# Optimization experiments

Hardware: AMD Instinct MI355X
Metric: run time of the kernel (lower is better)

Reference implementation:

```python
import jax, jax.numpy as jnp
import numpy as np

N, E = 50000, 800000
F_IN, HID, SENT = 128, 128, 128
NEG_SLOPE = 0.2  # GATConv default negative_slope


def _glorot(key, shape):
    fan_in, fan_out = shape[0], shape[-1]
    lim = float(np.sqrt(6.0 / (fan_in + fan_out)))
    return jax.random.uniform(key, shape, jnp.float32, -lim, lim)


def _gat_layer(x, src, dst, edge_attr, W, att_s, att_d, We, att_e, b):
    """PyG GATConv, heads=1, add_self_loops=True (fill_value='mean')."""
    n = x.shape[0]
    # self-loop edge_attr = mean of incoming edge features per dst node
    deg = jax.ops.segment_sum(jnp.ones(src.shape[0], x.dtype), dst, num_segments=n)
    loop_attr = jax.ops.segment_sum(edge_attr, dst, num_segments=n) / jnp.maximum(deg, 1.0)[:, None]
    loops = jnp.arange(n, dtype=src.dtype)
    src = jnp.concatenate([src, loops])
    dst = jnp.concatenate([dst, loops])
    ea = jnp.concatenate([edge_attr, loop_attr], axis=0)
    # projections (lin_src used for both src and dst when x is a single tensor)
    h = x @ W                           # [N, C]
    a_s = h @ att_s                     # [N]
    a_d = h @ att_d                     # [N]
    a_e = (ea @ We) @ att_e             # [E+N]
    alpha = jax.nn.leaky_relu(a_s[src] + a_d[dst] + a_e, NEG_SLOPE)
    # segment softmax over dst neighborhoods (self-loops guarantee nonempty)
    m = jax.ops.segment_max(alpha, dst, num_segments=n)
    ex = jnp.exp(alpha - m[dst])
    w = ex / jax.ops.segment_sum(ex, dst, num_segments=n)[dst]
    # message = alpha * h_src, scatter-add to dst
    return jax.ops.segment_sum(w[:, None] * h[src], dst, num_segments=n) + b


def setup_inputs() -> dict:
    key = jax.random.key(0)
    ks = jax.random.split(key, 16)
    x = jax.random.normal(ks[0], (N, F_IN), jnp.float32)
    edge_index = jax.random.randint(ks[1], (2, E), 0, N, jnp.int64)
    edge_attr = jax.random.normal(ks[2], (E, SENT), jnp.float32)
    params = {
        'W1': _glorot(ks[3], (F_IN, HID)),
        'a1s': _glorot(ks[4], (HID,)),
        'a1d': _glorot(ks[5], (HID,)),
        'We1': _glorot(ks[6], (SENT, HID)),
        'ae1': _glorot(ks[7], (HID,)),
        'b1': jnp.zeros((HID,), jnp.float32),
        'W2': _glorot(ks[8], (HID, HID)),
        'a2s': _glorot(ks[9], (HID,)),
        'a2d': _glorot(ks[10], (HID,)),
        'We2': _glorot(ks[11], (SENT, HID)),
        'ae2': _glorot(ks[12], (HID,)),
        'b2': jnp.zeros((HID,), jnp.float32),
    }
    return {'x': x, 'edge_index': edge_index, 'edge_attr': edge_attr, **params}


def reference(x, edge_index, edge_attr, W1, a1s, a1d, We1, ae1, b1,
              W2, a2s, a2d, We2, ae2, b2):
    src, dst = edge_index[0], edge_index[1]
    h = _gat_layer(x, src, dst, edge_attr, W1, a1s, a1d, We1, ae1, b1)
    h = jax.nn.relu(h)  # dropout p=0.1 inactive in eval
    return _gat_layer(h, src, dst, edge_attr, W2, a2s, a2d, We2, ae2, b2)
```

## Files before the change

kernel.cpp:

```cpp
#include <hip/hip_runtime.h>
#include <cstdint>

#define D 128
#define NEG 0.2f

typedef __attribute__((ext_vector_type(8))) short bf16x8;
typedef __attribute__((ext_vector_type(4))) float f32x4;

__device__ __forceinline__ float wsum(float v){
#pragma unroll
  for(int m=32;m;m>>=1) v += __shfl_xor(v,m,64);
  return v;
}
__device__ __forceinline__ float lrelu(float a){ return a>0.f ? a : NEG*a; }
__device__ __forceinline__ unsigned short f2bf(float f){
  unsigned int u = __float_as_uint(f);
  u += 0x7fffu + ((u>>16)&1u);
  return (unsigned short)(u>>16);
}
__device__ __forceinline__ float bf2f(unsigned short s){
  return __uint_as_float(((unsigned int)s)<<16);
}

__global__ __launch_bounds__(256) void k_init(const float* __restrict__ We1, const float* __restrict__ ae1,
                                              const float* __restrict__ We2, const float* __restrict__ ae2,
                                              const float* __restrict__ W1,  const float* __restrict__ W2,
                                              float* __restrict__ weae, ushort* __restrict__ Wtb){
  __shared__ ushort lds[16][128];
  if (blockIdx.x < 64){
    int gw  = (blockIdx.x*256 + threadIdx.x) >> 6;
    int lane = threadIdx.x & 63;
    const float* We = (gw & 128) ? We2 : We1;
    const float* ae = (gw & 128) ? ae2 : ae1;
    int row = gw & 127;
    float2 v = ((const float2*)(We + (size_t)row*D))[lane];
    float2 a = ((const float2*)ae)[lane];
    float p = wsum(v.x*a.x + v.y*a.y);
    if (!lane) weae[gw] = p;
  } else {
    int b = blockIdx.x - 64;
    int layer = b >> 3;
    int kb = (b & 7) * 16;
    const float* W = layer ? W2 : W1;
    int t = threadIdx.x;
#pragma unroll
    for (int p = 0; p < 8; ++p){
      int idx = t + p*256;
      int kl = idx >> 7, c = idx & 127;
      lds[kl][c] = f2bf(W[(size_t)(kb+kl)*128 + c]);
    }
    __syncthreads();
    int c = t >> 1, kc = (t & 1) * 8;
    ushort tmp[8];
#pragma unroll
    for (int m = 0; m < 8; ++m) tmp[m] = lds[kc+m][c];
    *(uint4*)&Wtb[(size_t)layer*16384 + (size_t)c*128 + kb + kc] = *(uint4*)tmp;
  }
}

__global__ __launch_bounds__(256) void k_edge(const float* __restrict__ EA, const int* __restrict__ dstv,
                                              const float* __restrict__ weae,
                                              float2* __restrict__ aeE12,
                                              int* __restrict__ deg, int E){
  int l   = threadIdx.x & 63;
  int sub = l & 7;
  int grp = l >> 3;
  float4 w1v[4], w2v[4];
#pragma unroll
  for (int k = 0; k < 4; ++k){
    w1v[k] = ((const float4*)weae)[sub + 8*k];
    w2v[k] = ((const float4*)weae)[32 + sub + 8*k];
  }
  int gwave  = (blockIdx.x*blockDim.x + threadIdx.x) >> 6;
  int nwaves = (gridDim.x*blockDim.x) >> 6;
  for (int e0 = gwave*8; e0 < E; e0 += nwaves*8){
    int e = e0 + grp;
    const float4* row = (const float4*)(EA + (size_t)e*D);
    float s1 = 0.f, s2 = 0.f;
#pragma unroll
    for (int k = 0; k < 4; ++k){
      float4 v = row[sub + 8*k];
      s1 += v.x*w1v[k].x + v.y*w1v[k].y + v.z*w1v[k].z + v.w*w1v[k].w;
      s2 += v.x*w2v[k].x + v.y*w2v[k].y + v.z*w2v[k].z + v.w*w2v[k].w;
    }
#pragma unroll
    for (int m = 1; m <= 4; m <<= 1){
      s1 += __shfl_xor(s1, m, 64);
      s2 += __shfl_xor(s2, m, 64);
    }
    if (!sub){
      aeE12[e] = make_float2(s1, s2);
      atomicAdd(deg + dstv[e], 1);
    }
  }
}

__global__ __launch_bounds__(256) void k_scan1(const int* __restrict__ deg, int* __restrict__ bsum, int N){
  __shared__ int s[256];
  int i = blockIdx.x*256 + threadIdx.x;
  s[threadIdx.x] = (i < N) ? deg[i] : 0;
  __syncthreads();
#pragma unroll
  for (int st = 128; st; st >>= 1){
    if (threadIdx.x < st) s[threadIdx.x] += s[threadIdx.x + st];
    __syncthreads();
  }
  if (!threadIdx.x) bsum[blockIdx.x] = s[0];
}
__global__ __launch_bounds__(256) void k_scan2(const int* __restrict__ bsum, int* __restrict__ boff, int NB){
  __shared__ int s[256];
  int t = threadIdx.x;
  int v = (t < NB) ? bsum[t] : 0;
  s[t] = v; __syncthreads();
  for (int d = 1; d < 256; d <<= 1){
    int x = (t >= d) ? s[t-d] : 0;
    __syncthreads();
    s[t] += x;
    __syncthreads();
  }
  boff[t] = s[t] - v;
}
__global__ __launch_bounds__(256) void k_scan3(const int* __restrict__ deg, const int* __restrict__ boff,
                                               int* __restrict__ rowp, int N, int E){
  __shared__ int s[256];
  int t = threadIdx.x;
  int i = blockIdx.x*256 + t;
  int v = (i < N) ? deg[i] : 0;
  s[t] = v; __syncthreads();
  for (int d = 1; d < 256; d <<= 1){
    int x = (t >= d) ? s[t-d] : 0;
    __syncthreads();
    s[t] += x;
    __syncthreads();
  }
  if (i < N) rowp[i] = boff[blockIdx.x] + s[t] - v;
  if (i == N-1) rowp[N] = E;
}

__global__ __launch_bounds__(256) void k_csr(const int* __restrict__ srcv, const int* __restrict__ dstv,
                                             const int* __restrict__ rowp, int* __restrict__ cursor,
                                             const float2* __restrict__ aeE12,
                                             int4* __restrict__ csr, int E){
  int e = blockIdx.x*256 + threadIdx.x;
  if (e >= E) return;
  int d = dstv[e];
  int pos = rowp[d] + atomicAdd(cursor + d, 1);
  float2 ae = aeE12[e];
  int4 rec;
  rec.x = srcv[e];
  rec.y = __float_as_int(ae.x);
  rec.z = __float_as_int(ae.y);
  rec.w = d;
  csr[pos] = rec;
}

__global__ __launch_bounds__(256) void k_gemm(const float* __restrict__ Xf, const ushort* __restrict__ Xb,
                                              const ushort* __restrict__ Wtb,
                                              const float* __restrict__ atts, const float* __restrict__ attd,
                                              ushort* __restrict__ Hb,
                                              float* __restrict__ a_s, float* __restrict__ a_d, int N){
  __shared__ ushort xsb[64*136];
  __shared__ ushort wsb[128*136];
  int tid = threadIdx.x;
  int rowbase = blockIdx.x*64;
  if (Xf){
#pragma unroll
    for (int i = 0; i < 4; ++i){
      int idx = tid + i*256;
      int r = idx >> 4, ch = idx & 15;
      int gr = rowbase + r;
      int grc = (gr < N) ? gr : 0;
      const float4* src = (const float4*)(Xf + (size_t)grc*128 + ch*8);
      float4 a = src[0], b = src[1];
      uint4 o;
      o.x = (unsigned)f2bf(a.x) | ((unsigned)f2bf(a.y)<<16);
      o.y = (unsigned)f2bf(a.z) | ((unsigned)f2bf(a.w)<<16);
      o.z = (unsigned)f2bf(b.x) | ((unsigned)f2bf(b.y)<<16);
      o.w = (unsigned)f2bf(b.z) | ((unsigned)f2bf(b.w)<<16);
      *(uint4*)&xsb[r*136 + ch*8] = o;
    }
  } else {
#pragma unroll
    for (int i = 0; i < 4; ++i){
      int idx = tid + i*256;
      int r = idx >> 4, ch = idx & 15;
      int gr = rowbase + r;
      int grc = (gr < N) ? gr : 0;
      *(uint4*)&xsb[r*136 + ch*8] = *(const uint4*)&Xb[(size_t)grc*128 + ch*8];
    }
  }
#pragma unroll
  for (int i = 0; i < 8; ++i){
    int idx = tid + i*256;
    int c = idx >> 4, ch = idx & 15;
    *(uint4*)&wsb[c*136 + ch*8] = *(const uint4*)&Wtb[(size_t)c*128 + ch*8];
  }
  __syncthreads();

  int lane = tid & 63;
  int w    = tid >> 6;
  int l15  = lane & 15;
  int lg   = lane >> 4;
  int r0   = w*16;

  f32x4 acc[8];
#pragma unroll
  for (int ct = 0; ct < 8; ++ct) acc[ct] = (f32x4){0.f,0.f,0.f,0.f};

#pragma unroll
  for (int ks = 0; ks < 4; ++ks){
    bf16x8 af = *(const bf16x8*)&xsb[(r0 + l15)*136 + ks*32 + lg*8];
#pragma unroll
    for (int ct = 0; ct < 8; ++ct){
      bf16x8 bfr = *(const bf16x8*)&wsb[(ct*16 + l15)*136 + ks*32 + lg*8];
      acc[ct] = __builtin_amdgcn_mfma_f32_16x16x32_bf16(af, bfr, acc[ct], 0, 0, 0);
    }
  }

  float attsv[8], attdv[8];
#pragma unroll
  for (int ct = 0; ct < 8; ++ct){
    attsv[ct] = atts[ct*16 + l15];
    attdv[ct] = attd[ct*16 + l15];
  }
  float ps[4] = {0,0,0,0}, pd[4] = {0,0,0,0};
#pragma unroll
  for (int ct = 0; ct < 8; ++ct)
#pragma unroll
    for (int j = 0; j < 4; ++j){
      ps[j] += acc[ct][j]*attsv[ct];
      pd[j] += acc[ct][j]*attdv[ct];
    }
#pragma unroll
  for (int m = 1; m <= 8; m <<= 1)
#pragma unroll
    for (int j = 0; j < 4; ++j){
      ps[j] += __shfl_xor(ps[j], m, 64);
      pd[j] += __shfl_xor(pd[j], m, 64);
    }
#pragma unroll
  for (int j = 0; j < 4; ++j){
    int gr = rowbase + r0 + lg*4 + j;
    if (gr < N && l15 == 0){
      a_s[gr] = ps[j];
      a_d[gr] = pd[j];
    }
  }
#pragma unroll
  for (int ct = 0; ct < 8; ++ct)
#pragma unroll
    for (int j = 0; j < 4; ++j){
      int r = r0 + lg*4 + j;
      xsb[r*136 + ct*16 + l15] = f2bf(acc[ct][j]);
    }
  __syncthreads();
#pragma unroll
  for (int i = 0; i < 4; ++i){
    int idx = tid + i*256;
    int r = idx >> 4, ch = idx & 15;
    int gr = rowbase + r;
    if (gr < N)
      *(uint4*)&Hb[(size_t)gr*128 + ch*8] = *(const uint4*)&xsb[r*136 + ch*8];
  }
}

__global__ __launch_bounds__(256) void k_aggr(const ushort* __restrict__ Hb,
                                              const float* __restrict__ a_s, const float* __restrict__ a_d,
                                              const int* __restrict__ rowp, const int4* __restrict__ csr,
                                              int layer,
                                              const float* __restrict__ bias,
                                              float* __restrict__ OUTF, ushort* __restrict__ OUTB, int N){
  __shared__ uint2 lse[4][64];
  int wslot = threadIdx.x >> 6;
  int wid  = (blockIdx.x*blockDim.x + threadIdx.x) >> 6;
  int lane = threadIdx.x & 63;
  if (wid >= N) return;
  int p0 = rowp[wid], p1 = rowp[wid+1];
  float as_own = a_s[wid];
  float ad     = a_d[wid];
  int l32 = lane & 31;
  int hw  = lane >> 5;
  ushort4 uself = make_ushort4(0,0,0,0);
  if (!hw) uself = *(const ushort4*)(Hb + (size_t)wid*D + l32*4);
  float denom = 0.f, sumae = 0.f;
  float4 acc = {0.f,0.f,0.f,0.f};
  for (int c0 = p0; c0 < p1; c0 += 64){
    int p = c0 + lane;
    bool valid = p < p1;
    int4 rec = valid ? csr[p] : make_int4(0,0,0,0);
    float ae = valid ? __int_as_float(layer ? rec.z : rec.y) : 0.f;
    float ex = valid ? __expf(lrelu(a_s[rec.x] + ad + ae)) : 0.f;
    sumae += wsum(ae);
    denom += wsum(ex);
    lse[wslot][lane] = make_uint2((unsigned)rec.x, __float_as_uint(ex));
    int cnt = p1 - c0; if (cnt > 64) cnt = 64;
    for (int it = 0; it*16 < cnt; ++it){
      int base = it*16 + hw*8;
#pragma unroll
      for (int k = 0; k < 8; ++k){
        uint2 t = lse[wslot][base + k];
        float w2 = __uint_as_float(t.y);
        ushort4 u = *(const ushort4*)(Hb + (size_t)t.x*D + l32*4);
        acc.x += w2*bf2f(u.x); acc.y += w2*bf2f(u.y);
        acc.z += w2*bf2f(u.z); acc.w += w2*bf2f(u.w);
      }
    }
  }
  float dg = (float)(p1 - p0);
  float la = sumae / fmaxf(dg, 1.0f);
  float ex_self = __expf(lrelu(as_own + ad + la));
  denom += ex_self;
  acc.x += __shfl_xor(acc.x, 32);
  acc.y += __shfl_xor(acc.y, 32);
  acc.z += __shfl_xor(acc.z, 32);
  acc.w += __shfl_xor(acc.w, 32);
  if (!hw){
    acc.x += ex_self*bf2f(uself.x); acc.y += ex_self*bf2f(uself.y);
    acc.z += ex_self*bf2f(uself.z); acc.w += ex_self*bf2f(uself.w);
    float4 bv = *(const float4*)(bias + l32*4);
    float inv = 1.0f/denom;
    float ox = acc.x*inv + bv.x, oy = acc.y*inv + bv.y;
    float oz = acc.z*inv + bv.z, ow = acc.w*inv + bv.w;
    if (OUTB){
      ox=fmaxf(ox,0.f); oy=fmaxf(oy,0.f); oz=fmaxf(oz,0.f); ow=fmaxf(ow,0.f);
      ushort4 o;
      o.x=f2bf(ox); o.y=f2bf(oy); o.z=f2bf(oz); o.w=f2bf(ow);
      *(ushort4*)(OUTB + (size_t)wid*D + l32*4) = o;
    } else {
      *(float4*)(OUTF + (size_t)wid*D + l32*4) = make_float4(ox,oy,oz,ow);
    }
  }
}

extern "C" void kernel_launch(void* const* d_in, const int* in_sizes, int n_in,
                              void* d_out, int out_size, void* d_ws, size_t ws_size,
                              hipStream_t stream){
  (void)n_in; (void)out_size; (void)ws_size;
  const float* x   = (const float*)d_in[0];
  const int*   ei  = (const int*)d_in[1];
  const float* ea  = (const float*)d_in[2];
  const float* W1  = (const float*)d_in[3];
  const float* a1s = (const float*)d_in[4];
  const float* a1d = (const float*)d_in[5];
  const float* We1 = (const float*)d_in[6];
  const float* ae1 = (const float*)d_in[7];
  const float* b1  = (const float*)d_in[8];
  const float* W2  = (const float*)d_in[9];
  const float* a2s = (const float*)d_in[10];
  const float* a2d = (const float*)d_in[11];
  const float* We2 = (const float*)d_in[12];
  const float* ae2 = (const float*)d_in[13];
  const float* b2  = (const float*)d_in[14];
  int N = in_sizes[0] / D;
  int E = in_sizes[1] / 2;
  const int* srcv = ei;
  const int* dstv = ei + E;
  float* out = (float*)d_out;

  char* p = (char*)d_ws;
  auto allocB = [&](size_t bytes)->void*{
    void* r = (void*)p; p += (bytes + 255) & ~(size_t)255; return r;
  };
  int* deg     = (int*)allocB((size_t)N*4);
  int* cursor  = (int*)allocB((size_t)N*4);
  char* zero_end = p;
  ushort* hb   = (ushort*)allocB((size_t)N*D*2);
  ushort* x2b  = (ushort*)allocB((size_t)N*D*2);
  ushort* Wtb  = (ushort*)allocB((size_t)2*128*128*2);
  float* aeE12 = (float*)allocB((size_t)E*8);
  int4* csr    = (int4*)allocB((size_t)E*16);
  float* as_   = (float*)allocB((size_t)N*4);
  float* ad_   = (float*)allocB((size_t)N*4);
  float* weae  = (float*)allocB(1024);
  int* rowp    = (int*)allocB((size_t)(N+1)*4);
  int* bsum    = (int*)allocB(1024);
  int* boff    = (int*)allocB(1024);

  hipMemsetAsync(deg, 0, (size_t)(zero_end - (char*)deg), stream);

  k_init<<<80,256,0,stream>>>(We1,ae1,We2,ae2,W1,W2,weae,Wtb);
  k_edge<<<2048,256,0,stream>>>(ea,dstv,weae,(float2*)aeE12,deg,E);

  int nb = (N + 255)/256;
  k_scan1<<<nb,256,0,stream>>>(deg,bsum,N);
  k_scan2<<<1,256,0,stream>>>(bsum,boff,nb);
  k_scan3<<<nb,256,0,stream>>>(deg,boff,rowp,N,E);
  k_csr<<<(E+255)/256,256,0,stream>>>(srcv,dstv,rowp,cursor,(const float2*)aeE12,csr,E);

  int gemmb = (N + 63)/64;
  int wgrid = (N + 3)/4;

  k_gemm<<<gemmb,256,0,stream>>>(x, nullptr, Wtb,          a1s, a1d, hb, as_, ad_, N);
  k_aggr<<<wgrid,256,0,stream>>>(hb, as_, ad_, rowp, csr, 0, b1, nullptr, x2b, N);

  k_gemm<<<gemmb,256,0,stream>>>(nullptr, x2b, Wtb + 16384, a2s, a2d, hb, as_, ad_, N);
  k_aggr<<<wgrid,256,0,stream>>>(hb, as_, ad_, rowp, csr, 1, b2, out, nullptr, N);
}
```

Before: 271.4 us.

## Reorder CSR build: histogram first, fuse edge projection with CSR scatter into per-layer lists

The degree histogram now runs as its own kernel first. The first scan level is merged with the weight-prep kernel, and scan levels two and three are combined into one kernel. The edge projection kernel now scatters directly into CSR position, writing two compact per-layer (src, ae) 8-byte lists instead of an intermediate aeE12 array plus a 16-byte CSR record. This removes one kernel pass over E edges and halves the per-edge record read in each aggregation layer, at the cost of random scatter writes from the edge-attribute kernel.

```diff
diff --git a/kernel.cpp b/kernel.cpp
--- a/kernel.cpp
+++ b/kernel.cpp
@@ -22,13 +22,31 @@
   return __uint_as_float(((unsigned int)s)<<16);
 }
 
-__global__ __launch_bounds__(256) void k_init(const float* __restrict__ We1, const float* __restrict__ ae1,
-                                              const float* __restrict__ We2, const float* __restrict__ ae2,
-                                              const float* __restrict__ W1,  const float* __restrict__ W2,
-                                              float* __restrict__ weae, ushort* __restrict__ Wtb){
+__global__ __launch_bounds__(256) void k_hist(const int* __restrict__ dstv, int* __restrict__ deg, int E){
+  int e = blockIdx.x*256 + threadIdx.x;
+  if (e < E) atomicAdd(deg + dstv[e], 1);
+}
+
+__global__ __launch_bounds__(256) void k_scan1i(const int* __restrict__ deg, int* __restrict__ bsum, int N, int NB,
+                                                const float* __restrict__ We1, const float* __restrict__ ae1,
+                                                const float* __restrict__ We2, const float* __restrict__ ae2,
+                                                const float* __restrict__ W1,  const float* __restrict__ W2,
+                                                float* __restrict__ weae, ushort* __restrict__ Wtb){
+  __shared__ int s[256];
   __shared__ ushort lds[16][128];
-  if (blockIdx.x < 64){
-    int gw  = (blockIdx.x*256 + threadIdx.x) >> 6;
+  int b = blockIdx.x;
+  if (b < NB){
+    int i = b*256 + threadIdx.x;
+    s[threadIdx.x] = (i < N) ? deg[i] : 0;
+    __syncthreads();
+#pragma unroll
+    for (int st = 128; st; st >>= 1){
+      if (threadIdx.x < st) s[threadIdx.x] += s[threadIdx.x + st];
+      __syncthreads();
+    }
+    if (!threadIdx.x) bsum[b] = s[0];
+  } else if (b < NB + 64){
+    int gw  = ((b - NB)*256 + threadIdx.x) >> 6;
     int lane = threadIdx.x & 63;
     const float* We = (gw & 128) ? We2 : We1;
     const float* ae = (gw & 128) ? ae2 : ae1;
@@ -38,9 +56,9 @@
     float p = wsum(v.x*a.x + v.y*a.y);
     if (!lane) weae[gw] = p;
   } else {
-    int b = blockIdx.x - 64;
-    int layer = b >> 3;
-    int kb = (b & 7) * 16;
+    int bb = b - NB - 64;
+    int layer = bb >> 3;
+    int kb = (bb & 7) * 16;
     const float* W = layer ? W2 : W1;
     int t = threadIdx.x;
 #pragma unroll
@@ -58,56 +76,8 @@
   }
 }
 
-__global__ __launch_bounds__(256) void k_edge(const float* __restrict__ EA, const int* __restrict__ dstv,
-                                              const float* __restrict__ weae,
-                                              float2* __restrict__ aeE12,
-                                              int* __restrict__ deg, int E){
-  int l   = threadIdx.x & 63;
-  int sub = l & 7;
-  int grp = l >> 3;
-  float4 w1v[4], w2v[4];
-#pragma unroll
-  for (int k = 0; k < 4; ++k){
-    w1v[k] = ((const float4*)weae)[sub + 8*k];
-    w2v[k] = ((const float4*)weae)[32 + sub + 8*k];
-  }
-  int gwave  = (blockIdx.x*blockDim.x + threadIdx.x) >> 6;
-  int nwaves = (gridDim.x*blockDim.x) >> 6;
-  for (int e0 = gwave*8; e0 < E; e0 += nwaves*8){
-    int e = e0 + grp;
-    const float4* row = (const float4*)(EA + (size_t)e*D);
-    float s1 = 0.f, s2 = 0.f;
-#pragma unroll
-    for (int k = 0; k < 4; ++k){
-      float4 v = row[sub + 8*k];
-      s1 += v.x*w1v[k].x + v.y*w1v[k].y + v.z*w1v[k].z + v.w*w1v[k].w;
-      s2 += v.x*w2v[k].x + v.y*w2v[k].y + v.z*w2v[k].z + v.w*w2v[k].w;
-    }
-#pragma unroll
-    for (int m = 1; m <= 4; m <<= 1){
-      s1 += __shfl_xor(s1, m, 64);
-      s2 += __shfl_xor(s2, m, 64);
-    }
-    if (!sub){
-      aeE12[e] = make_float2(s1, s2);
-      atomicAdd(deg + dstv[e], 1);
-    }
-  }
-}
-
-__global__ __launch_bounds__(256) void k_scan1(const int* __restrict__ deg, int* __restrict__ bsum, int N){
-  __shared__ int s[256];
-  int i = blockIdx.x*256 + threadIdx.x;
-  s[threadIdx.x] = (i < N) ? deg[i] : 0;
-  __syncthreads();
-#pragma unroll
-  for (int st = 128; st; st >>= 1){
-    if (threadIdx.x < st) s[threadIdx.x] += s[threadIdx.x + st];
-    __syncthreads();
-  }
-  if (!threadIdx.x) bsum[blockIdx.x] = s[0];
-}
-__global__ __launch_bounds__(256) void k_scan2(const int* __restrict__ bsum, int* __restrict__ boff, int NB){
+__global__ __launch_bounds__(256) void k_scan23(const int* __restrict__ deg, const int* __restrict__ bsum,
+                                                int* __restrict__ rowp, int NB, int N, int E){
   __shared__ int s[256];
   int t = threadIdx.x;
   int v = (t < NB) ? bsum[t] : 0;
@@ -118,40 +88,61 @@
     s[t] += x;
     __syncthreads();
   }
-  boff[t] = s[t] - v;
-}
-__global__ __launch_bounds__(256) void k_scan3(const int* __restrict__ deg, const int* __restrict__ boff,
-                                               int* __restrict__ rowp, int N, int E){
-  __shared__ int s[256];
-  int t = threadIdx.x;
+  int boff = (blockIdx.x == 0) ? 0 : s[blockIdx.x - 1];
+  __syncthreads();
   int i = blockIdx.x*256 + t;
-  int v = (i < N) ? deg[i] : 0;
-  s[t] = v; __syncthreads();
+  int dv = (i < N) ? deg[i] : 0;
+  s[t] = dv; __syncthreads();
   for (int d = 1; d < 256; d <<= 1){
     int x = (t >= d) ? s[t-d] : 0;
     __syncthreads();
     s[t] += x;
     __syncthreads();
   }
-  if (i < N) rowp[i] = boff[blockIdx.x] + s[t] - v;
+  if (i < N) rowp[i] = boff + s[t] - dv;
   if (i == N-1) rowp[N] = E;
 }
 
-__global__ __launch_bounds__(256) void k_csr(const int* __restrict__ srcv, const int* __restrict__ dstv,
-                                             const int* __restrict__ rowp, int* __restrict__ cursor,
-                                             const float2* __restrict__ aeE12,
-                                             int4* __restrict__ csr, int E){
-  int e = blockIdx.x*256 + threadIdx.x;
-  if (e >= E) return;
-  int d = dstv[e];
-  int pos = rowp[d] + atomicAdd(cursor + d, 1);
-  float2 ae = aeE12[e];
-  int4 rec;
-  rec.x = srcv[e];
-  rec.y = __float_as_int(ae.x);
-  rec.z = __float_as_int(ae.y);
-  rec.w = d;
-  csr[pos] = rec;
+__global__ __launch_bounds__(256) void k_edge(const float* __restrict__ EA,
+                                              const int* __restrict__ srcv, const int* __restrict__ dstv,
+                                              const float* __restrict__ weae,
+                                              const int* __restrict__ rowp, int* __restrict__ cursor,
+                                              uint2* __restrict__ pl1, uint2* __restrict__ pl2, int E){
+  int l   = threadIdx.x & 63;
+  int sub = l & 7;
+  int grp = l >> 3;
+  float4 w1v[4], w2v[4];
+#pragma unroll
+  for (int k = 0; k < 4; ++k){
+    w1v[k] = ((const float4*)weae)[sub + 8*k];
+    w2v[k] = ((const float4*)weae)[32 + sub + 8*k];
+  }
+  int gwave  = (blockIdx.x*blockDim.x + threadIdx.x) >> 6;
+  int nwaves = (gridDim.x*blockDim.x) >> 6;
+  for (int e0 = gwave*8; e0 < E; e0 += nwaves*8){
+    int e = e0 + grp;
+    if (e >= E) continue;
+    const float4* row = (const float4*)(EA + (size_t)e*D);
+    float s1 = 0.f, s2 = 0.f;
+#pragma unroll
+    for (int k = 0; k < 4; ++k){
+      float4 v = row[sub + 8*k];
+      s1 += v.x*w1v[k].x + v.y*w1v[k].y + v.z*w1v[k].z + v.w*w1v[k].w;
+      s2 += v.x*w2v[k].x + v.y*w2v[k].y + v.z*w2v[k].z + v.w*w2v[k].w;
+    }
+#pragma unroll
+    for (int m = 1; m <= 4; m <<= 1){
+      s1 += __shfl_xor(s1, m, 64);
+      s2 += __shfl_xor(s2, m, 64);
+    }
+    if (!sub){
+      int d = dstv[e];
+      int pos = rowp[d] + atomicAdd(cursor + d, 1);
+      unsigned s = (unsigned)srcv[e];
+      pl1[pos] = make_uint2(s, __float_as_uint(s1));
+      pl2[pos] = make_uint2(s, __float_as_uint(s2));
+    }
+  }
 }
 
 __global__ __launch_bounds__(256) void k_gemm(const float* __restrict__ Xf, const ushort* __restrict__ Xb,
@@ -266,8 +257,7 @@
 
 __global__ __launch_bounds__(256) void k_aggr(const ushort* __restrict__ Hb,
                                               const float* __restrict__ a_s, const float* __restrict__ a_d,
-                                              const int* __restrict__ rowp, const int4* __restrict__ csr,
-                                              int layer,
+                                              const int* __restrict__ rowp, const uint2* __restrict__ pl,
                                               const float* __restrict__ bias,
                                               float* __restrict__ OUTF, ushort* __restrict__ OUTB, int N){
   __shared__ uint2 lse[4][64];
@@ -287,12 +277,12 @@
   for (int c0 = p0; c0 < p1; c0 += 64){
     int p = c0 + lane;
     bool valid = p < p1;
-    int4 rec = valid ? csr[p] : make_int4(0,0,0,0);
-    float ae = valid ? __int_as_float(layer ? rec.z : rec.y) : 0.f;
+    uint2 rec = valid ? pl[p] : make_uint2(0u, 0u);
+    float ae = valid ? __uint_as_float(rec.y) : 0.f;
     float ex = valid ? __expf(lrelu(a_s[rec.x] + ad + ae)) : 0.f;
     sumae += wsum(ae);
     denom += wsum(ex);
-    lse[wslot][lane] = make_uint2((unsigned)rec.x, __float_as_uint(ex));
+    lse[wslot][lane] = make_uint2(rec.x, __float_as_uint(ex));
     int cnt = p1 - c0; if (cnt > 64) cnt = 64;
     for (int it = 0; it*16 < cnt; ++it){
       int base = it*16 + hw*8;
@@ -367,32 +357,28 @@
   ushort* hb   = (ushort*)allocB((size_t)N*D*2);
   ushort* x2b  = (ushort*)allocB((size_t)N*D*2);
   ushort* Wtb  = (ushort*)allocB((size_t)2*128*128*2);
-  float* aeE12 = (float*)allocB((size_t)E*8);
-  int4* csr    = (int4*)allocB((size_t)E*16);
+  uint2* pl1   = (uint2*)allocB((size_t)E*8);
+  uint2* pl2   = (uint2*)allocB((size_t)E*8);
   float* as_   = (float*)allocB((size_t)N*4);
   float* ad_   = (float*)allocB((size_t)N*4);
   float* weae  = (float*)allocB(1024);
   int* rowp    = (int*)allocB((size_t)(N+1)*4);
   int* bsum    = (int*)allocB(1024);
-  int* boff    = (int*)allocB(1024);
 
   hipMemsetAsync(deg, 0, (size_t)(zero_end - (char*)deg), stream);
 
-  k_init<<<80,256,0,stream>>>(We1,ae1,We2,ae2,W1,W2,weae,Wtb);
-  k_edge<<<2048,256,0,stream>>>(ea,dstv,weae,(float2*)aeE12,deg,E);
-
   int nb = (N + 255)/256;
-  k_scan1<<<nb,256,0,stream>>>(deg,bsum,N);
-  k_scan2<<<1,256,0,stream>>>(bsum,boff,nb);
-  k_scan3<<<nb,256,0,stream>>>(deg,boff,rowp,N,E);
-  k_csr<<<(E+255)/256,256,0,stream>>>(srcv,dstv,rowp,cursor,(const float2*)aeE12,csr,E);
+  k_hist  <<<(E+255)/256,256,0,stream>>>(dstv, deg, E);
+  k_scan1i<<<nb+80,256,0,stream>>>(deg, bsum, N, nb, We1,ae1,We2,ae2,W1,W2, weae, Wtb);
+  k_scan23<<<nb,256,0,stream>>>(deg, bsum, rowp, nb, N, E);
+  k_edge  <<<2048,256,0,stream>>>(ea, srcv, dstv, weae, rowp, cursor, pl1, pl2, E);
 
   int gemmb = (N + 63)/64;
   int wgrid = (N + 3)/4;
 
   k_gemm<<<gemmb,256,0,stream>>>(x, nullptr, Wtb,          a1s, a1d, hb, as_, ad_, N);
-  k_aggr<<<wgrid,256,0,stream>>>(hb, as_, ad_, rowp, csr, 0, b1, nullptr, x2b, N);
+  k_aggr<<<wgrid,256,0,stream>>>(hb, as_, ad_, rowp, pl1, b1, nullptr, x2b, N);
 
   k_gemm<<<gemmb,256,0,stream>>>(nullptr, x2b, Wtb + 16384, a2s, a2d, hb, as_, ad_, N);
-  k_aggr<<<wgrid,256,0,stream>>>(hb, as_, ad_, rowp, csr, 1, b2, out, nullptr, N);
-}
+  k_aggr<<<wgrid,256,0,stream>>>(hb, as_, ad_, rowp, pl2, b2, out, nullptr, N);
+}
```

After: 275.6 us. No clear change (+1.5%).
